# Performance work log

Measured on AMD Instinct MI355X. Metric: run time of the kernel, lower is better.

Reference implementation:

```python
import jax, jax.numpy as jnp
import numpy as np

H = 768
NH = 12
HD = H // NH  # 64


def setup_inputs() -> dict:
    key = jax.random.key(0)
    ks = jax.random.split(key, 8)
    B, S = 4, 2048
    sc = 1.0 / np.sqrt(H)
    return {
        "hidden_states": jax.random.normal(ks[0], (B, S, H), dtype=jnp.float32),
        "attention_mask": jnp.zeros((B, 1, 1, S), dtype=jnp.float32),
        "Wq": jax.random.normal(ks[1], (H, H), dtype=jnp.float32) * sc,
        "bq": jnp.zeros((H,), dtype=jnp.float32),
        "Wk": jax.random.normal(ks[2], (H, H), dtype=jnp.float32) * sc,
        "bk": jnp.zeros((H,), dtype=jnp.float32),
        "Wv": jax.random.normal(ks[3], (H, H), dtype=jnp.float32) * sc,
        "bv": jnp.zeros((H,), dtype=jnp.float32),
    }


def _split_heads(x):
    # [B,S,H] -> [B,NH,S,HD]
    B, S, _ = x.shape
    return x.reshape(B, S, NH, HD).transpose(0, 2, 1, 3)


def reference(hidden_states, attention_mask, Wq, bq, Wk, bk, Wv, bv):
    q = _split_heads(hidden_states @ Wq + bq)
    k = _split_heads(hidden_states @ Wk + bk)
    v = _split_heads(hidden_states @ Wv + bv)
    # scores: [B,NH,S,S]
    scores = jnp.einsum("bhqd,bhkd->bhqk", q, k) / np.sqrt(HD)
    scores = scores + attention_mask
    probs = jax.nn.softmax(scores, axis=-1)  # dropout is identity in eval
    ctx = jnp.einsum("bhqk,bhkd->bhqd", probs, v)
    B, _, S, _ = ctx.shape
    return ctx.transpose(0, 2, 1, 3).reshape(B, S, H)
```

## Files before the change

kernel.cpp:

```cpp
#include <hip/hip_runtime.h>
#include <stdint.h>

typedef short bf16x8 __attribute__((ext_vector_type(8)));
typedef float f32x4  __attribute__((ext_vector_type(4)));
typedef unsigned short u16;

#define B_  4
#define S_  2048
#define H_  768
#define NH_ 12
#define HD_ 64
#define NPROJ_N (3*H_)
#define PSW 72

static __device__ __forceinline__ u16 f2bf(float f) {
    union { float f; unsigned int u; } x; x.f = f;
    return (u16)((x.u + 0x8000u) >> 16);
}
static __device__ __forceinline__ bf16x8 ld8(const u16* p) {
    return *(const bf16x8*)(const void*)p;
}
static __device__ __forceinline__ void st8(u16* p, bf16x8 v) {
    *(bf16x8*)(void*)p = v;
}
static __device__ __forceinline__ void async_ld16(const u16* g, const short* l) {
    __builtin_amdgcn_global_load_lds(
        (__attribute__((address_space(1))) void*)g,
        (__attribute__((address_space(3))) void*)l,
        16, 0, 0);
}

__global__ __launch_bounds__(256) void prep_kernel(const float* __restrict__ in,
                                                   u16* __restrict__ out,
                                                   const float* __restrict__ wq,
                                                   const float* __restrict__ wk,
                                                   const float* __restrict__ wv,
                                                   u16* __restrict__ wt) {
    __shared__ float t[32][33];
    const int blk = blockIdx.x;
    const int tid = threadIdx.x;
    if (blk < 6144) {
        int i = (blk * 256 + tid) * 4;
        float4 v = *(const float4*)(in + i);
        ushort4 o;
        o.x = f2bf(v.x); o.y = f2bf(v.y); o.z = f2bf(v.z); o.w = f2bf(v.w);
        *(ushort4*)(out + i) = o;
    } else {
        const int idx  = blk - 6144;
        const int proj = idx / 576;
        const int rem  = idx % 576;
        const int bx = rem % 24, by = rem / 24;
        const float* w = (proj == 0) ? wq : (proj == 1) ? wk : wv;
        u16* o = wt + (size_t)proj * H_ * H_;
        const int tx = tid & 31, ty = tid >> 5;
        const int n0 = bx * 32, k0 = by * 32;
        #pragma unroll
        for (int i = 0; i < 4; i++)
            t[ty + i * 8][tx] = w[(size_t)(k0 + ty + i * 8) * H_ + n0 + tx];
        __syncthreads();
        #pragma unroll
        for (int i = 0; i < 4; i++)
            o[(size_t)(n0 + ty + i * 8) * H_ + k0 + tx] = f2bf(t[tx][ty + i * 8]);
    }
}

__global__ __launch_bounds__(256) void qkv_gemm(const u16* __restrict__ A,
                                                const u16* __restrict__ Wt,
                                                const float* __restrict__ bq,
                                                const float* __restrict__ bk,
                                                const float* __restrict__ bv,
                                                u16* __restrict__ qo,
                                                u16* __restrict__ ko,
                                                u16* __restrict__ vto) {
    __shared__ alignas(16) short SMEM[4][128 * 64];

    const int tid  = threadIdx.x;
    const int wave = tid >> 6;
    const int lane = tid & 63;
    const int quad = lane >> 4;
    const int l16  = lane & 15;
    const int wm   = wave & 1;
    const int wn   = wave >> 1;

    const int id  = blockIdx.x;
    const int xcd = id & 7;
    const int j   = id >> 3;
    const int mi  = j & 7;
    const int ni  = j >> 3;
    const int m0 = (xcd * 8 + mi) * 128;
    const int n0 = ni * 128;

    int stR[4], stC[4];
    #pragma unroll
    for (int jj = 0; jj < 4; jj++) {
        const int lc = wave * 256 + jj * 64 + lane;
        stR[jj] = lc >> 3;
        stC[jj] = ((lc & 7) ^ (stR[jj] & 7)) * 8;
    }
    const int fx0 = (quad ^ (l16 & 7)) * 8;
    const int fx1 = fx0 ^ 32;

    f32x4 acc[4][4];
    #pragma unroll
    for (int i = 0; i < 4; i++)
        #pragma unroll
        for (int jj = 0; jj < 4; jj++) acc[i][jj] = (f32x4)0.0f;

#define GSTAGE(kt_, buf_)                                                                     \
    do {                                                                                      \
        const int kk_ = (kt_) * 64;                                                           \
        _Pragma("unroll")                                                                     \
        for (int jj = 0; jj < 4; jj++) {                                                      \
            async_ld16(A  + (size_t)(m0 + stR[jj]) * H_ + kk_ + stC[jj],                      \
                       &SMEM[(buf_) * 2][(wave * 256 + jj * 64) * 8]);                        \
            async_ld16(Wt + (size_t)(n0 + stR[jj]) * H_ + kk_ + stC[jj],                      \
                       &SMEM[(buf_) * 2 + 1][(wave * 256 + jj * 64) * 8]);                    \
        }                                                                                     \
    } while (0)

    GSTAGE(0, 0);
    __syncthreads();

    for (int kt = 0; kt < 12; kt++) {
        const int cur = kt & 1;
        if (kt + 1 < 12) GSTAGE(kt + 1, cur ^ 1);
        const short* As = SMEM[cur * 2];
        const short* Bs = SMEM[cur * 2 + 1];
        #pragma unroll
        for (int ks = 0; ks < 2; ks++) {
            const int fx = ks ? fx1 : fx0;
            bf16x8 af[4], bfr[4];
            #pragma unroll
            for (int i = 0; i < 4; i++)
                af[i] = *(const bf16x8*)(const void*)&As[(wm * 64 + i * 16 + l16) * 64 + fx];
            #pragma unroll
            for (int jj = 0; jj < 4; jj++)
                bfr[jj] = *(const bf16x8*)(const void*)&Bs[(wn * 64 + jj * 16 + l16) * 64 + fx];
            #pragma unroll
            for (int i = 0; i < 4; i++)
                #pragma unroll
                for (int jj = 0; jj < 4; jj++)
                    acc[i][jj] = __builtin_amdgcn_mfma_f32_16x16x32_bf16(af[i], bfr[jj], acc[i][jj], 0, 0, 0);
        }
        __syncthreads();
    }
#undef GSTAGE

    const int proj  = n0 / H_;
    const int hbase = (n0 % H_) >> 6;
    const float* bias = (proj == 0) ? bq : (proj == 1) ? bk : bv;
    u16* Ct = (u16*)SMEM;

    #pragma unroll
    for (int nj = 0; nj < 4; nj++) {
        const int nl = wn * 64 + nj * 16 + l16;
        const float bv_ = bias[(n0 % H_) + nl];
        #pragma unroll
        for (int mi2 = 0; mi2 < 4; mi2++) {
            #pragma unroll
            for (int r = 0; r < 4; r++) {
                const int ml = wm * 64 + mi2 * 16 + quad * 4 + r;
                const u16 val = f2bf(acc[mi2][nj][r] + bv_);
                if (proj < 2)
                    Ct[ml * 128 + ((nl + (ml & 15) * 8) & 127)] = val;
                else
                    Ct[nl * 128 + ((ml + (nl & 15) * 8) & 127)] = val;
            }
        }
    }
    __syncthreads();

    if (proj < 2) {
        u16* dst0 = (proj == 0) ? qo : ko;
        const int c = tid & 7;
        #pragma unroll
        for (int jj = 0; jj < 8; jj++) {
            const int idx = jj * 32 + (tid >> 3);
            const int ml = idx >> 1, h2 = idx & 1;
            const int nbase = h2 * 64 + c * 8;
            bf16x8 v8 = *(const bf16x8*)(const void*)&Ct[ml * 128 + ((nbase + (ml & 15) * 8) & 127)];
            const int m = m0 + ml;
            const int b = m >> 11, s = m & 2047;
            st8(dst0 + ((size_t)(b * NH_ + hbase + h2) * S_ + s) * HD_ + c * 8, v8);
        }
    } else {
        const int b = m0 >> 11;
        #pragma unroll
        for (int jj = 0; jj < 8; jj++) {
            const int nl = (tid >> 3) + (jj & 3) * 32;
            const int c  = (tid & 7) + (jj >> 2) * 8;
            bf16x8 v8 = *(const bf16x8*)(const void*)&Ct[nl * 128 + ((c * 8 + (nl & 15) * 8) & 127)];
            const int h2 = nl >> 6, d = nl & 63;
            st8(vto + ((size_t)(b * NH_ + hbase + h2) * HD_ + d) * S_ + (m0 & 2047) + c * 8, v8);
        }
    }
}

__global__ __launch_bounds__(512) void attn_kernel(const u16* __restrict__ q,
                                                   const u16* __restrict__ k,
                                                   const u16* __restrict__ vt,
                                                   const float* __restrict__ mask,
                                                   float* __restrict__ out) {
    __shared__ alignas(16) short Ks[2][64 * 64];
    __shared__ alignas(16) short Vs[2][64 * 64];
    __shared__ alignas(16) short Ps[128 * PSW];

    const int tid  = threadIdx.x;
    const int wave = tid >> 6;
    const int lane = tid & 63;
    const int quad = lane >> 4;
    const int l16  = lane & 15;

    const int bh = blockIdx.x;
    const int b  = bh / NH_;
    const int q0 = blockIdx.y * 128;
    const float C1 = 0.125f * 1.44269504f;

    const u16* qbase = q + ((size_t)bh * S_ + q0 + wave * 16 + l16) * HD_;
    bf16x8 qf0 = ld8(qbase + quad * 8);
    bf16x8 qf1 = ld8(qbase + 32 + quad * 8);

    const u16* kbase = k  + (size_t)bh * S_ * HD_;
    const u16* vbase = vt + (size_t)bh * HD_ * S_;

    const int sRow = tid >> 3;
    const int sCol = ((tid & 7) ^ (sRow & 7)) * 8;
    const int kOff = sRow * 64 + sCol;
    const int fx0 = (quad ^ (l16 & 7)) * 8;
    const int fx1 = fx0 ^ 32;

    float lsum[4] = {0.f, 0.f, 0.f, 0.f};
    f32x4 o_acc[4];
    #pragma unroll
    for (int c = 0; c < 4; c++) o_acc[c] = (f32x4)0.0f;

#define STAGE(kt_, buf_)                                                              \
    do {                                                                              \
        async_ld16(kbase + (size_t)(kt_) * 4096 + kOff,        &Ks[buf_][wave * 512]); \
        async_ld16(vbase + (size_t)sRow * S_ + (kt_) * 64 + sCol, &Vs[buf_][wave * 512]); \
    } while (0)

    STAGE(0, 0);
    __syncthreads();

    for (int kt = 0; kt < S_ / 64; kt++) {
        const int cur = kt & 1;
        if (kt + 1 < S_ / 64) STAGE(kt + 1, cur ^ 1);
        const int kk = kt * 64;
        const short* Kc = Ks[cur];
        const short* Vc = Vs[cur];

        f32x4 sacc[4];
        #pragma unroll
        for (int c = 0; c < 4; c++) sacc[c] = (f32x4)0.0f;
        #pragma unroll
        for (int c = 0; c < 4; c++) {
            bf16x8 kf0 = *(const bf16x8*)(const void*)&Kc[(c * 16 + l16) * 64 + fx0];
            sacc[c] = __builtin_amdgcn_mfma_f32_16x16x32_bf16(qf0, kf0, sacc[c], 0, 0, 0);
            bf16x8 kf1 = *(const bf16x8*)(const void*)&Kc[(c * 16 + l16) * 64 + fx1];
            sacc[c] = __builtin_amdgcn_mfma_f32_16x16x32_bf16(qf1, kf1, sacc[c], 0, 0, 0);
        }

        float pv[4][4];
        #pragma unroll
        for (int c = 0; c < 4; c++) {
            const float ml = mask[(size_t)b * S_ + kk + c * 16 + l16] * 1.44269504f;
            #pragma unroll
            for (int r = 0; r < 4; r++) {
                const float p = __builtin_amdgcn_exp2f(sacc[c][r] * C1 + ml);
                pv[c][r] = p;
                lsum[r] += p;
            }
        }

        u16* Pw = (u16*)Ps;
        #pragma unroll
        for (int c = 0; c < 4; c++)
            #pragma unroll
            for (int r = 0; r < 4; r++)
                Pw[(wave * 16 + quad * 4 + r) * PSW + c * 16 + l16] = f2bf(pv[c][r]);

        bf16x8 pa0 = *(const bf16x8*)(const void*)&Ps[(wave * 16 + l16) * PSW + quad * 8];
        bf16x8 pa1 = *(const bf16x8*)(const void*)&Ps[(wave * 16 + l16) * PSW + 32 + quad * 8];
        #pragma unroll
        for (int c2 = 0; c2 < 4; c2++) {
            bf16x8 vb0 = *(const bf16x8*)(const void*)&Vc[(c2 * 16 + l16) * 64 + fx0];
            o_acc[c2] = __builtin_amdgcn_mfma_f32_16x16x32_bf16(pa0, vb0, o_acc[c2], 0, 0, 0);
            bf16x8 vb1 = *(const bf16x8*)(const void*)&Vc[(c2 * 16 + l16) * 64 + fx1];
            o_acc[c2] = __builtin_amdgcn_mfma_f32_16x16x32_bf16(pa1, vb1, o_acc[c2], 0, 0, 0);
        }
        __syncthreads();
    }
#undef STAGE

    const int h = bh % NH_;
    #pragma unroll
    for (int r = 0; r < 4; r++) {
        float l = lsum[r];
        #pragma unroll
        for (int off = 1; off < 16; off <<= 1) l += __shfl_xor(l, off);
        const float linv = 1.0f / l;
        const int s = q0 + wave * 16 + quad * 4 + r;
        #pragma unroll
        for (int c2 = 0; c2 < 4; c2++) {
            const int d = c2 * 16 + l16;
            out[((size_t)b * S_ + s) * H_ + h * 64 + d] = o_acc[c2][r] * linv;
        }
    }
}

extern "C" void kernel_launch(void* const* d_in, const int* in_sizes, int n_in,
                              void* d_out, int out_size, void* d_ws, size_t ws_size,
                              hipStream_t stream) {
    const float* hidden = (const float*)d_in[0];
    const float* amask  = (const float*)d_in[1];
    const float* Wq     = (const float*)d_in[2];
    const float* bq     = (const float*)d_in[3];
    const float* Wk     = (const float*)d_in[4];
    const float* bk     = (const float*)d_in[5];
    const float* Wv     = (const float*)d_in[6];
    const float* bv     = (const float*)d_in[7];
    float* out = (float*)d_out;

    char* ws = (char*)d_ws;
    const size_t sz_hidden = (size_t)B_ * S_ * H_ * 2;
    const size_t sz_wt     = (size_t)NPROJ_N * H_ * 2;
    const size_t sz_qkv    = (size_t)B_ * S_ * H_ * 2;

    u16* hid_bf = (u16*)(ws);
    u16* wt     = (u16*)(ws + sz_hidden);
    u16* qbuf   = (u16*)(ws + sz_hidden + sz_wt);
    u16* kbuf   = (u16*)(ws + sz_hidden + sz_wt + sz_qkv);
    u16* vtbuf  = (u16*)(ws + sz_hidden + sz_wt + 2 * sz_qkv);

    prep_kernel<<<dim3(6144 + 1728), dim3(256), 0, stream>>>(
        hidden, hid_bf, Wq, Wk, Wv, wt);
    qkv_gemm<<<dim3(1152), dim3(256), 0, stream>>>(
        hid_bf, wt, bq, bk, bv, qbuf, kbuf, vtbuf);
    attn_kernel<<<dim3(B_ * NH_, S_ / 128), dim3(512), 0, stream>>>(
        qbuf, kbuf, vtbuf, amask, out);
}
```

Before: 212.9 us.

## Enlarge QKV GEMM tiles, swizzle P buffer, compute row sums via MFMA

The QKV GEMM moves to 256x128 tiles with 512 threads and a single LDS buffer that has sync before and after each load, which drops the old double buffering. Its epilogue now runs in two halves and uses nontemporal stores. In attention, the padded P buffer becomes an XOR-swizzled 64-wide layout. Softmax row sums now come from an MFMA against a ones vector instead of per-lane adds plus shuffles, and the output also uses nontemporal stores. The aim is more data reuse per tile, fewer LDS bank conflicts and fewer VALU/shuffle ops. The cost is lost load/compute overlap in the GEMM, and row sums are now taken from bf16-rounded P.

```diff
diff --git a/kernel.cpp b/kernel.cpp
--- a/kernel.cpp
+++ b/kernel.cpp
@@ -11,7 +11,6 @@
 #define NH_ 12
 #define HD_ 64
 #define NPROJ_N (3*H_)
-#define PSW 72
 
 static __device__ __forceinline__ u16 f2bf(float f) {
     union { float f; unsigned int u; } x; x.f = f;
@@ -20,8 +19,8 @@
 static __device__ __forceinline__ bf16x8 ld8(const u16* p) {
     return *(const bf16x8*)(const void*)p;
 }
-static __device__ __forceinline__ void st8(u16* p, bf16x8 v) {
-    *(bf16x8*)(void*)p = v;
+static __device__ __forceinline__ void st8nt(u16* p, bf16x8 v) {
+    __builtin_nontemporal_store(v, (bf16x8*)(void*)p);
 }
 static __device__ __forceinline__ void async_ld16(const u16* g, const short* l) {
     __builtin_amdgcn_global_load_lds(
@@ -64,7 +63,7 @@
     }
 }
 
-__global__ __launch_bounds__(256) void qkv_gemm(const u16* __restrict__ A,
+__global__ __launch_bounds__(512) void qkv_gemm(const u16* __restrict__ A,
                                                 const u16* __restrict__ Wt,
                                                 const float* __restrict__ bq,
                                                 const float* __restrict__ bk,
@@ -72,30 +71,36 @@
                                                 u16* __restrict__ qo,
                                                 u16* __restrict__ ko,
                                                 u16* __restrict__ vto) {
-    __shared__ alignas(16) short SMEM[4][128 * 64];
+    __shared__ alignas(16) short SMEM[24576];
+    short* As = SMEM;
+    short* Bs = SMEM + 16384;
 
     const int tid  = threadIdx.x;
     const int wave = tid >> 6;
     const int lane = tid & 63;
     const int quad = lane >> 4;
     const int l16  = lane & 15;
-    const int wm   = wave & 1;
-    const int wn   = wave >> 1;
+    const int wm   = wave & 3;
+    const int wn   = wave >> 2;
 
     const int id  = blockIdx.x;
     const int xcd = id & 7;
     const int j   = id >> 3;
-    const int mi  = j & 7;
-    const int ni  = j >> 3;
-    const int m0 = (xcd * 8 + mi) * 128;
-    const int n0 = ni * 128;
-
-    int stR[4], stC[4];
-    #pragma unroll
-    for (int jj = 0; jj < 4; jj++) {
-        const int lc = wave * 256 + jj * 64 + lane;
-        stR[jj] = lc >> 3;
-        stC[jj] = ((lc & 7) ^ (stR[jj] & 7)) * 8;
+    const int m0  = (xcd * 4 + (j & 3)) * 256;
+    const int n0  = (j >> 2) * 128;
+
+    int aR[4], aC[4], bR[2], bC[2];
+    #pragma unroll
+    for (int ja = 0; ja < 4; ja++) {
+        const int lc = wave * 256 + ja * 64 + lane;
+        aR[ja] = lc >> 3;
+        aC[ja] = ((lc & 7) ^ (aR[ja] & 7)) * 8;
+    }
+    #pragma unroll
+    for (int jb = 0; jb < 2; jb++) {
+        const int lc = wave * 128 + jb * 64 + lane;
+        bR[jb] = lc >> 3;
+        bC[jb] = ((lc & 7) ^ (bR[jb] & 7)) * 8;
     }
     const int fx0 = (quad ^ (l16 & 7)) * 8;
     const int fx1 = fx0 ^ 32;
@@ -106,26 +111,18 @@
         #pragma unroll
         for (int jj = 0; jj < 4; jj++) acc[i][jj] = (f32x4)0.0f;
 
-#define GSTAGE(kt_, buf_)                                                                     \
-    do {                                                                                      \
-        const int kk_ = (kt_) * 64;                                                           \
-        _Pragma("unroll")                                                                     \
-        for (int jj = 0; jj < 4; jj++) {                                                      \
-            async_ld16(A  + (size_t)(m0 + stR[jj]) * H_ + kk_ + stC[jj],                      \
-                       &SMEM[(buf_) * 2][(wave * 256 + jj * 64) * 8]);                        \
-            async_ld16(Wt + (size_t)(n0 + stR[jj]) * H_ + kk_ + stC[jj],                      \
-                       &SMEM[(buf_) * 2 + 1][(wave * 256 + jj * 64) * 8]);                    \
-        }                                                                                     \
-    } while (0)
-
-    GSTAGE(0, 0);
-    __syncthreads();
-
     for (int kt = 0; kt < 12; kt++) {
-        const int cur = kt & 1;
-        if (kt + 1 < 12) GSTAGE(kt + 1, cur ^ 1);
-        const short* As = SMEM[cur * 2];
-        const short* Bs = SMEM[cur * 2 + 1];
+        const int kk = kt * 64;
+        __syncthreads();
+        #pragma unroll
+        for (int ja = 0; ja < 4; ja++)
+            async_ld16(A + (size_t)(m0 + aR[ja]) * H_ + kk + aC[ja],
+                       &As[wave * 2048 + ja * 512]);
+        #pragma unroll
+        for (int jb = 0; jb < 2; jb++)
+            async_ld16(Wt + (size_t)(n0 + bR[jb]) * H_ + kk + bC[jb],
+                       &Bs[wave * 1024 + jb * 512]);
+        __syncthreads();
         #pragma unroll
         for (int ks = 0; ks < 2; ks++) {
             const int fx = ks ? fx1 : fx0;
@@ -142,56 +139,59 @@
                 for (int jj = 0; jj < 4; jj++)
                     acc[i][jj] = __builtin_amdgcn_mfma_f32_16x16x32_bf16(af[i], bfr[jj], acc[i][jj], 0, 0, 0);
         }
-        __syncthreads();
-    }
-#undef GSTAGE
+    }
 
     const int proj  = n0 / H_;
     const int hbase = (n0 % H_) >> 6;
     const float* bias = (proj == 0) ? bq : (proj == 1) ? bk : bv;
+    const int b = m0 >> 11;
     u16* Ct = (u16*)SMEM;
 
     #pragma unroll
-    for (int nj = 0; nj < 4; nj++) {
-        const int nl = wn * 64 + nj * 16 + l16;
-        const float bv_ = bias[(n0 % H_) + nl];
-        #pragma unroll
-        for (int mi2 = 0; mi2 < 4; mi2++) {
-            #pragma unroll
-            for (int r = 0; r < 4; r++) {
-                const int ml = wm * 64 + mi2 * 16 + quad * 4 + r;
-                const u16 val = f2bf(acc[mi2][nj][r] + bv_);
-                if (proj < 2)
-                    Ct[ml * 128 + ((nl + (ml & 15) * 8) & 127)] = val;
-                else
-                    Ct[nl * 128 + ((ml + (nl & 15) * 8) & 127)] = val;
+    for (int half = 0; half < 2; half++) {
+        __syncthreads();
+        if ((wm >> 1) == half) {
+            const int mlBase = (wm & 1) * 64;
+            #pragma unroll
+            for (int nj = 0; nj < 4; nj++) {
+                const int nl = wn * 64 + nj * 16 + l16;
+                const float bv_ = bias[(n0 % H_) + nl];
+                #pragma unroll
+                for (int mi2 = 0; mi2 < 4; mi2++) {
+                    #pragma unroll
+                    for (int r = 0; r < 4; r++) {
+                        const int ml = mlBase + mi2 * 16 + quad * 4 + r;
+                        const u16 val = f2bf(acc[mi2][nj][r] + bv_);
+                        if (proj < 2)
+                            Ct[ml * 128 + ((nl + (ml & 15) * 8) & 127)] = val;
+                        else
+                            Ct[nl * 128 + ((ml + (nl & 15) * 8) & 127)] = val;
+                    }
+                }
             }
         }
-    }
-    __syncthreads();
-
-    if (proj < 2) {
-        u16* dst0 = (proj == 0) ? qo : ko;
-        const int c = tid & 7;
-        #pragma unroll
-        for (int jj = 0; jj < 8; jj++) {
-            const int idx = jj * 32 + (tid >> 3);
-            const int ml = idx >> 1, h2 = idx & 1;
-            const int nbase = h2 * 64 + c * 8;
-            bf16x8 v8 = *(const bf16x8*)(const void*)&Ct[ml * 128 + ((nbase + (ml & 15) * 8) & 127)];
-            const int m = m0 + ml;
-            const int b = m >> 11, s = m & 2047;
-            st8(dst0 + ((size_t)(b * NH_ + hbase + h2) * S_ + s) * HD_ + c * 8, v8);
-        }
-    } else {
-        const int b = m0 >> 11;
-        #pragma unroll
-        for (int jj = 0; jj < 8; jj++) {
-            const int nl = (tid >> 3) + (jj & 3) * 32;
-            const int c  = (tid & 7) + (jj >> 2) * 8;
-            bf16x8 v8 = *(const bf16x8*)(const void*)&Ct[nl * 128 + ((c * 8 + (nl & 15) * 8) & 127)];
-            const int h2 = nl >> 6, d = nl & 63;
-            st8(vto + ((size_t)(b * NH_ + hbase + h2) * HD_ + d) * S_ + (m0 & 2047) + c * 8, v8);
+        __syncthreads();
+        if (proj < 2) {
+            u16* dst0 = (proj == 0) ? qo : ko;
+            const int c = tid & 7;
+            #pragma unroll
+            for (int jj = 0; jj < 4; jj++) {
+                const int idx = jj * 64 + (tid >> 3);
+                const int ml = idx >> 1, h2 = idx & 1;
+                bf16x8 v8 = *(const bf16x8*)(const void*)&Ct[ml * 128 + (((h2 * 64 + c * 8) + (ml & 15) * 8) & 127)];
+                const int s = (m0 + half * 128 + ml) & 2047;
+                st8nt(dst0 + ((size_t)(b * NH_ + hbase + h2) * S_ + s) * HD_ + c * 8, v8);
+            }
+        } else {
+            const int s0 = (m0 + half * 128) & 2047;
+            #pragma unroll
+            for (int jj = 0; jj < 4; jj++) {
+                const int nl = (tid >> 3) + (jj & 1) * 64;
+                const int c  = (tid & 7) + (jj >> 1) * 8;
+                bf16x8 v8 = *(const bf16x8*)(const void*)&Ct[nl * 128 + ((c * 8 + (nl & 15) * 8) & 127)];
+                const int h2 = nl >> 6, d = nl & 63;
+                st8nt(vto + ((size_t)(b * NH_ + hbase + h2) * HD_ + d) * S_ + s0 + c * 8, v8);
+            }
         }
     }
 }
@@ -203,7 +203,7 @@
                                                    float* __restrict__ out) {
     __shared__ alignas(16) short Ks[2][64 * 64];
     __shared__ alignas(16) short Vs[2][64 * 64];
-    __shared__ alignas(16) short Ps[128 * PSW];
+    __shared__ alignas(16) short Ps[128 * 64];
 
     const int tid  = threadIdx.x;
     const int wave = tid >> 6;
@@ -228,15 +228,19 @@
     const int kOff = sRow * 64 + sCol;
     const int fx0 = (quad ^ (l16 & 7)) * 8;
     const int fx1 = fx0 ^ 32;
-
-    float lsum[4] = {0.f, 0.f, 0.f, 0.f};
+    const int l16l = l16 & 7, l16h = l16 >> 3;
+
+    const short one_bf = (short)0x3F80;
+    const bf16x8 bones = {one_bf, one_bf, one_bf, one_bf, one_bf, one_bf, one_bf, one_bf};
+
     f32x4 o_acc[4];
+    f32x4 lacc = (f32x4)0.0f;
     #pragma unroll
     for (int c = 0; c < 4; c++) o_acc[c] = (f32x4)0.0f;
 
 #define STAGE(kt_, buf_)                                                              \
     do {                                                                              \
-        async_ld16(kbase + (size_t)(kt_) * 4096 + kOff,        &Ks[buf_][wave * 512]); \
+        async_ld16(kbase + (size_t)(kt_) * 4096 + kOff,           &Ks[buf_][wave * 512]); \
         async_ld16(vbase + (size_t)sRow * S_ + (kt_) * 64 + sCol, &Vs[buf_][wave * 512]); \
     } while (0)
 
@@ -261,27 +265,24 @@
             sacc[c] = __builtin_amdgcn_mfma_f32_16x16x32_bf16(qf1, kf1, sacc[c], 0, 0, 0);
         }
 
-        float pv[4][4];
+        u16* Pw = (u16*)Ps;
         #pragma unroll
         for (int c = 0; c < 4; c++) {
             const float ml = mask[(size_t)b * S_ + kk + c * 16 + l16] * 1.44269504f;
             #pragma unroll
             for (int r = 0; r < 4; r++) {
                 const float p = __builtin_amdgcn_exp2f(sacc[c][r] * C1 + ml);
-                pv[c][r] = p;
-                lsum[r] += p;
+                const int row = wave * 16 + quad * 4 + r;
+                const int ch  = (2 * c + l16h) ^ (row & 7);
+                Pw[row * 64 + ch * 8 + l16l] = f2bf(p);
             }
         }
 
-        u16* Pw = (u16*)Ps;
-        #pragma unroll
-        for (int c = 0; c < 4; c++)
-            #pragma unroll
-            for (int r = 0; r < 4; r++)
-                Pw[(wave * 16 + quad * 4 + r) * PSW + c * 16 + l16] = f2bf(pv[c][r]);
-
-        bf16x8 pa0 = *(const bf16x8*)(const void*)&Ps[(wave * 16 + l16) * PSW + quad * 8];
-        bf16x8 pa1 = *(const bf16x8*)(const void*)&Ps[(wave * 16 + l16) * PSW + 32 + quad * 8];
+        const int prow = wave * 16 + l16;
+        bf16x8 pa0 = *(const bf16x8*)(const void*)&Ps[prow * 64 + fx0];
+        bf16x8 pa1 = *(const bf16x8*)(const void*)&Ps[prow * 64 + fx1];
+        lacc = __builtin_amdgcn_mfma_f32_16x16x32_bf16(pa0, bones, lacc, 0, 0, 0);
+        lacc = __builtin_amdgcn_mfma_f32_16x16x32_bf16(pa1, bones, lacc, 0, 0, 0);
         #pragma unroll
         for (int c2 = 0; c2 < 4; c2++) {
             bf16x8 vb0 = *(const bf16x8*)(const void*)&Vc[(c2 * 16 + l16) * 64 + fx0];
@@ -296,15 +297,13 @@
     const int h = bh % NH_;
     #pragma unroll
     for (int r = 0; r < 4; r++) {
-        float l = lsum[r];
-        #pragma unroll
-        for (int off = 1; off < 16; off <<= 1) l += __shfl_xor(l, off);
-        const float linv = 1.0f / l;
+        const float linv = 1.0f / lacc[r];
         const int s = q0 + wave * 16 + quad * 4 + r;
         #pragma unroll
         for (int c2 = 0; c2 < 4; c2++) {
             const int d = c2 * 16 + l16;
-            out[((size_t)b * S_ + s) * H_ + h * 64 + d] = o_acc[c2][r] * linv;
+            __builtin_nontemporal_store(o_acc[c2][r] * linv,
+                                        &out[((size_t)b * S_ + s) * H_ + h * 64 + d]);
         }
     }
 }
@@ -335,7 +334,7 @@
 
     prep_kernel<<<dim3(6144 + 1728), dim3(256), 0, stream>>>(
         hidden, hid_bf, Wq, Wk, Wv, wt);
-    qkv_gemm<<<dim3(1152), dim3(256), 0, stream>>>(
+    qkv_gemm<<<dim3(576), dim3(512), 0, stream>>>(
         hid_bf, wt, bq, bk, bv, qbuf, kbuf, vtbuf);
     attn_kernel<<<dim3(B_ * NH_, S_ / 128), dim3(512), 0, stream>>>(
         qbuf, kbuf, vtbuf, amask, out);
```

After: 250.9 us. +17.9%, slower.
